# Kernel optimization log

Hardware: AMD Instinct MI355X
Metric: run time of the kernel (lower is better)

The kernel has to match this reference:

```python
import jax, jax.numpy as jnp
import numpy as np

B, N = 1, 1024
C_A, C_Z, H = 768, 128, 16
CH = C_A // H  # 48
INV_SQRT_CH = float(1.0 / np.sqrt(CH))


def _ln(x, w, b):
    # torch.nn.LayerNorm over last dim, eps=1e-5
    m = jnp.mean(x, axis=-1, keepdims=True)
    v = jnp.mean(jnp.square(x - m), axis=-1, keepdims=True)
    return (x - m) * jax.lax.rsqrt(v + 1e-5) * w + b


def setup_inputs() -> dict:
    key = jax.random.key(0)
    ks = jax.random.split(key, 8)
    rn = lambda k, shape, sc: jax.random.normal(k, shape, dtype=jnp.float32) * sc
    return {
        "a": rn(ks[0], (B, N, C_A), 1.0),
        "z": rn(ks[1], (B, N, N, C_Z), 1.0),
        "mask": jnp.ones((B, N), dtype=jnp.float32),
        "ln_a_w": jnp.ones((C_A,), jnp.float32),
        "ln_a_b": jnp.zeros((C_A,), jnp.float32),
        "ln_z_w": jnp.ones((C_Z,), jnp.float32),
        "ln_z_b": jnp.zeros((C_Z,), jnp.float32),
        "Wq": rn(ks[2], (C_A, H * CH), 0.02),
        "bq": jnp.zeros((H * CH,), jnp.float32),
        "Wk": rn(ks[3], (C_A, H * CH), 0.02),
        "Wv": rn(ks[4], (C_A, H * CH), 0.02),
        "Wb": rn(ks[5], (C_Z, H), 0.02),
        "Wg": rn(ks[6], (C_A, H * CH), 0.02),
        "Wo": rn(ks[7], (H * CH, C_A), 0.02),
    }


def reference(a, z, mask, ln_a_w, ln_a_b, ln_z_w, ln_z_b, Wq, bq, Wk, Wv, Wb, Wg, Wo):
    an = _ln(a, ln_a_w, ln_a_b)                                  # [B, N, C_A]
    q = (an @ Wq + bq).reshape(B, N, H, CH)
    k = (an @ Wk).reshape(B, N, H, CH)
    v = (an @ Wv).reshape(B, N, H, CH)
    # pair bias: LayerNorm(z) -> per-head scalar bias [B, N, N, H]
    bpair = _ln(z, ln_z_w, ln_z_b) @ Wb
    mbias = (mask - 1.0)[:, None, None, :] * 1e9                  # [B, 1, 1, N]
    logits = jnp.einsum('bqhc,bkhc->bhqk', q, k) * INV_SQRT_CH
    logits = logits + jnp.transpose(bpair, (0, 3, 1, 2)) + mbias  # [B, H, N, N]
    attn = jax.nn.softmax(logits, axis=-1)
    o = jnp.einsum('bhqk,bkhc->bqhc', attn, v)                    # [B, N, H, CH]
    g = jax.nn.sigmoid(an @ Wg).reshape(B, N, H, CH)
    out = (g * o).reshape(B, N, H * CH) @ Wo                      # [B, N, C_A]
    return out
```

## Files before the change

kernel.cpp:

```cpp
#include <hip/hip_runtime.h>

#define NSEQ 1024
#define CA   768
#define CZ   128
#define NH   16
#define CHD  48
#define HC   768
#define INV_SQRT_CH 0.14433756729740643f

typedef float v4f __attribute__((ext_vector_type(4)));
typedef short v8s __attribute__((ext_vector_type(8)));

__device__ __forceinline__ short f2bf(float f) {
  union { float f; unsigned u; } v; v.f = f;
  unsigned r = v.u + 0x7fffu + ((v.u >> 16) & 1u);
  return (short)(r >> 16);
}
__device__ __forceinline__ float bf2f(short s) {
  union { unsigned u; float f; } v;
  v.u = ((unsigned)(unsigned short)s) << 16;
  return v.f;
}
__device__ __forceinline__ unsigned cvtpk(float lo, float hi) {
  unsigned r;
  asm("v_cvt_pk_bf16_f32 %0, %1, %2" : "=v"(r) : "v"(lo), "v"(hi));
  return r;
}

__global__ __launch_bounds__(256) void k_front(
    const float* __restrict__ lnzw, const float* __restrict__ lnzb,
    const float* __restrict__ Wb, short* __restrict__ wWp, float* __restrict__ S1bW,
    const float* __restrict__ Wq, const float* __restrict__ Wk,
    const float* __restrict__ Wv, const float* __restrict__ Wg,
    const float* __restrict__ Wo, short* __restrict__ WT, short* __restrict__ WoT,
    const float* __restrict__ a, const float* __restrict__ lnaw,
    const float* __restrict__ lnab, short* __restrict__ anb)
{
  __shared__ __align__(16) char fsm[64 * 65 * 4];
  const int bid = blockIdx.x;
  const int t = threadIdx.x;

  if (bid == 0) {
    const int s = t >> 6, l = t & 63;
    const int r16 = l & 15, cg = l >> 4;
    float v[8];
    #pragma unroll
    for (int j = 0; j < 8; ++j) {
      int d = s * 32 + cg * 8 + j;
      v[j] = lnzw[d] * Wb[d * NH + r16];
    }
    uint4 pk;
    pk.x = cvtpk(v[0], v[1]); pk.y = cvtpk(v[2], v[3]);
    pk.z = cvtpk(v[4], v[5]); pk.w = cvtpk(v[6], v[7]);
    *(uint4*)(wWp + (s * 64 + l) * 8) = pk;
    if (t < NH) {
      float s1 = 0.f, bw = 0.f;
      for (int d = 0; d < CZ; ++d) {
        float wb = Wb[d * NH + t];
        s1 += bf2f(f2bf(lnzw[d] * wb));
        bw += lnzb[d] * wb;
      }
      S1bW[t] = s1;
      S1bW[NH + t] = bw;
    }
  } else if (bid <= 720) {
    float (*tile)[65] = (float(*)[65])fsm;
    const int cb = bid - 1;
    const int mat = cb / 144, rem = cb % 144;
    const int tk = rem % 12, tn = rem / 12;
    const int k0 = tk * 64, n0 = tn * 64;
    const float* __restrict__ W =
        (mat == 0) ? Wq : (mat == 1) ? Wk : (mat == 2) ? Wv : (mat == 3) ? Wg : Wo;
    const float s = (mat == 0) ? INV_SQRT_CH : 1.f;
    const int rr = t >> 4, cc = (t & 15) * 4;
    #pragma unroll
    for (int r = 0; r < 4; ++r) {
      v4f v = *(const v4f*)(W + (size_t)(k0 + r * 16 + rr) * HC + n0 + cc);
      tile[r * 16 + rr][cc + 0] = v[0];
      tile[r * 16 + rr][cc + 1] = v[1];
      tile[r * 16 + rr][cc + 2] = v[2];
      tile[r * 16 + rr][cc + 3] = v[3];
    }
    __syncthreads();
    short* dst = (mat < 4) ? (WT + (size_t)mat * HC * CA) : WoT;
    #pragma unroll
    for (int r = 0; r < 4; ++r) {
      const int nr = r * 16 + rr;
      uint2 pk;
      pk.x = cvtpk(tile[cc + 0][nr] * s, tile[cc + 1][nr] * s);
      pk.y = cvtpk(tile[cc + 2][nr] * s, tile[cc + 3][nr] * s);
      *(uint2*)(dst + (size_t)(n0 + nr) * CA + k0 + cc) = pk;
    }
  } else {
    float* red = (float*)fsm;
    const int row = bid - 721;
    const float* ar = a + (size_t)row * CA;
    float x[3];
    float s = 0.f, s2 = 0.f;
    #pragma unroll
    for (int i = 0; i < 3; ++i) {
      x[i] = ar[t + i * 256];
      s += x[i]; s2 += x[i] * x[i];
    }
    #pragma unroll
    for (int off = 1; off < 64; off <<= 1) {
      s += __shfl_xor(s, off);
      s2 += __shfl_xor(s2, off);
    }
    const int wv = t >> 6;
    if ((t & 63) == 0) { red[wv] = s; red[4 + wv] = s2; }
    __syncthreads();
    s = red[0] + red[1] + red[2] + red[3];
    s2 = red[4] + red[5] + red[6] + red[7];
    const float m = s * (1.f / CA);
    const float var = s2 * (1.f / CA) - m * m;
    const float rs = rsqrtf(var + 1e-5f);
    #pragma unroll
    for (int i = 0; i < 3; ++i) {
      int c = t + i * 256;
      anb[(size_t)row * CA + c] = f2bf((x[i] - m) * rs * lnaw[c] + lnab[c]);
    }
  }
}

__global__ __launch_bounds__(256) void k23_fused(
    const short* __restrict__ anb, const short* __restrict__ WT,
    const float* __restrict__ bq, const float* __restrict__ z,
    const short* __restrict__ wWp, const float* __restrict__ S1bW,
    short* __restrict__ qb, short* __restrict__ kb, short* __restrict__ vT,
    float* __restrict__ gbuf, short* __restrict__ bpair)
{
  __shared__ __align__(16) char smem[20480];
  const int tid = threadIdx.x;
  const int w = tid >> 6, l = tid & 63;
  const int r16 = l & 15, cg = l >> 4;

  if (blockIdx.x < 192) {
    const int bid = blockIdx.x;
    const int bm = bid & 7;
    const int bnb = bid >> 3;
    const int m0 = bm * 128, n0 = bnb * 128;
    const int wr = w >> 1, wc = w & 1;

    short* As = (short*)smem;
    short* Bs = (short*)(smem + 10240);

    const int strow = w * 16 + (l >> 2);
    const int scol = (l & 3) * 8;

    v4f acc[4][4];
    #pragma unroll
    for (int i = 0; i < 4; ++i)
      #pragma unroll
      for (int j = 0; j < 4; ++j)
        acc[i][j] = (v4f){0.f, 0.f, 0.f, 0.f};

    for (int k0 = 0; k0 < CA; k0 += 32) {
      v8s av0 = *(const v8s*)(anb + (size_t)(m0 + strow) * CA + k0 + scol);
      v8s av1 = *(const v8s*)(anb + (size_t)(m0 + 64 + strow) * CA + k0 + scol);
      v8s bv0 = *(const v8s*)(WT + (size_t)(n0 + strow) * CA + k0 + scol);
      v8s bv1 = *(const v8s*)(WT + (size_t)(n0 + 64 + strow) * CA + k0 + scol);
      __syncthreads();
      *(v8s*)(As + (size_t)strow * 40 + scol) = av0;
      *(v8s*)(As + (size_t)(64 + strow) * 40 + scol) = av1;
      *(v8s*)(Bs + (size_t)strow * 40 + scol) = bv0;
      *(v8s*)(Bs + (size_t)(64 + strow) * 40 + scol) = bv1;
      __syncthreads();
      v8s a[4], b[4];
      #pragma unroll
      for (int m = 0; m < 4; ++m)
        a[m] = *(const v8s*)(As + (wr * 64 + m * 16 + r16) * 40 + cg * 8);
      #pragma unroll
      for (int n = 0; n < 4; ++n)
        b[n] = *(const v8s*)(Bs + (wc * 64 + n * 16 + r16) * 40 + cg * 8);
      #pragma unroll
      for (int m = 0; m < 4; ++m)
        #pragma unroll
        for (int n = 0; n < 4; ++n)
          acc[m][n] = __builtin_amdgcn_mfma_f32_16x16x32_bf16(a[m], b[n], acc[m][n], 0, 0, 0);
    }

    const int matsel = n0 / HC;
    #pragma unroll
    for (int n = 0; n < 4; ++n) {
      const int nc = (n0 % HC) + wc * 64 + n * 16 + r16;
      const int rbase = m0 + wr * 64 + cg * 4;
      if (matsel == 0) {
        const float bqs = bq[nc] * INV_SQRT_CH;
        #pragma unroll
        for (int m = 0; m < 4; ++m)
          #pragma unroll
          for (int j = 0; j < 4; ++j)
            qb[(size_t)(rbase + m * 16 + j) * HC + nc] = f2bf(acc[m][n][j] + bqs);
      } else if (matsel == 1) {
        #pragma unroll
        for (int m = 0; m < 4; ++m)
          #pragma unroll
          for (int j = 0; j < 4; ++j)
            kb[(size_t)(rbase + m * 16 + j) * HC + nc] = f2bf(acc[m][n][j]);
      } else if (matsel == 2) {
        #pragma unroll
        for (int m = 0; m < 4; ++m) {
          uint2 pk;
          pk.x = cvtpk(acc[m][n][0], acc[m][n][1]);
          pk.y = cvtpk(acc[m][n][2], acc[m][n][3]);
          *(uint2*)(vT + (size_t)nc * NSEQ + rbase + m * 16) = pk;
        }
      } else {
        #pragma unroll
        for (int m = 0; m < 4; ++m)
          #pragma unroll
          for (int j = 0; j < 4; ++j)
            gbuf[(size_t)(rbase + m * 16 + j) * HC + nc] =
                1.f / (1.f + __expf(-acc[m][n][j]));
      }
    }
  } else {
    const int zbid = blockIdx.x - 192;
    const int q = zbid >> 4;
    const int k0 = (zbid & 15) << 6;
    short* blds = (short*)smem;

    v8s bfrag[4];
    #pragma unroll
    for (int s = 0; s < 4; ++s) bfrag[s] = *(const v8s*)(wWp + (s * 64 + l) * 8);
    const float S1 = S1bW[r16];
    const float bW = S1bW[NH + r16];

    const int krow = k0 + w * 16 + r16;
    const float* __restrict__ zr = z + ((size_t)q * NSEQ + krow) * CZ;
    float sum = 0.f, sum2 = 0.f;
    v8s afrag[4];
    #pragma unroll
    for (int s = 0; s < 4; ++s) {
      v4f z0 = *(const v4f*)(zr + s * 32 + cg * 8);
      v4f z1 = *(const v4f*)(zr + s * 32 + cg * 8 + 4);
      #pragma unroll
      for (int j = 0; j < 4; ++j) {
        sum += z0[j] + z1[j];
        sum2 += z0[j] * z0[j] + z1[j] * z1[j];
      }
      union { v8s s8; unsigned u[4]; } fu;
      fu.u[0] = cvtpk(z0[0], z0[1]);
      fu.u[1] = cvtpk(z0[2], z0[3]);
      fu.u[2] = cvtpk(z1[0], z1[1]);
      fu.u[3] = cvtpk(z1[2], z1[3]);
      afrag[s] = fu.s8;
    }
    sum  += __shfl_xor(sum, 16);  sum  += __shfl_xor(sum, 32);
    sum2 += __shfl_xor(sum2, 16); sum2 += __shfl_xor(sum2, 32);
    const float mean = sum * (1.f / CZ);
    const float var = sum2 * (1.f / CZ) - mean * mean;
    const float rs = rsqrtf(var + 1e-5f);

    v4f acc = {0.f, 0.f, 0.f, 0.f};
    #pragma unroll
    for (int s = 0; s < 4; ++s)
      acc = __builtin_amdgcn_mfma_f32_16x16x32_bf16(afrag[s], bfrag[s], acc, 0, 0, 0);

    float bv[4];
    #pragma unroll
    for (int j = 0; j < 4; ++j) {
      int src = cg * 4 + j;
      float mj = __shfl(mean, src);
      float rj = __shfl(rs, src);
      bv[j] = rj * (acc[j] - mj * S1) + bW;
    }
    uint2 bu;
    bu.x = cvtpk(bv[0], bv[1]);
    bu.y = cvtpk(bv[2], bv[3]);
    *(uint2*)&blds[r16 * 72 + w * 16 + cg * 4] = bu;
    __syncthreads();
    const int h = tid >> 4, kk = (tid & 15) << 2;
    uint2 v = *(const uint2*)&blds[h * 72 + kk];
    *(uint2*)(bpair + (size_t)h * NSEQ * NSEQ + (size_t)q * NSEQ + k0 + kk) = v;
  }
}

#define PL_STRIDE 136
#define BL_STRIDE 144
__global__ __launch_bounds__(256) void k4_attn(
    const short* __restrict__ qb, const short* __restrict__ kb,
    const short* __restrict__ vT, const short* __restrict__ bpair,
    const float* __restrict__ mask,
    float* __restrict__ po, float* __restrict__ pm, float* __restrict__ plo)
{
  const int h = blockIdx.x & 15;
  const int qt = (blockIdx.x >> 4) & 15;
  const int ks = blockIdx.x >> 8;
  const int tid = threadIdx.x;
  const int w = tid >> 6, l = tid & 63;
  const int r16 = l & 15, cg = l >> 4;
  const int q0 = qt * 64 + w * 16;
  const int kstart = ks * 256;

  __shared__ __align__(16) short plds[4][16 * PL_STRIDE];
  __shared__ __align__(16) short blds[4][16 * BL_STRIDE];
  short* pl = &plds[w][0];
  short* bl = &blds[w][0];

  const v8s vzero = {0, 0, 0, 0, 0, 0, 0, 0};
  v8s qf0, qf1;
  {
    const short* qp = qb + (size_t)(q0 + r16) * HC + h * CHD;
    qf0 = *(const v8s*)(qp + cg * 8);
    qf1 = (cg < 2) ? *(const v8s*)(qp + 32 + cg * 8) : vzero;
  }
  v4f of0 = {0, 0, 0, 0}, of1 = {0, 0, 0, 0}, of2 = {0, 0, 0, 0};
  float mrun[4], lrun[4];
  #pragma unroll
  for (int j = 0; j < 4; ++j) { mrun[j] = -1e30f; lrun[j] = 0.f; }

  const size_t bpb = (size_t)h * NSEQ * NSEQ;
  const int srow = l >> 2;
  const int scol = (l & 3) * 32;

  #pragma unroll
  for (int ch = 0; ch < 2; ++ch) {
    const int k0 = kstart + ch * 128;

    {
      const short* bsrc = bpair + bpb + (size_t)(q0 + srow) * NSEQ + k0 + scol;
      short* bdst = bl + srow * BL_STRIDE + scol;
      v8s t0 = *(const v8s*)(bsrc);
      v8s t1 = *(const v8s*)(bsrc + 8);
      v8s t2 = *(const v8s*)(bsrc + 16);
      v8s t3 = *(const v8s*)(bsrc + 24);
      *(v8s*)(bdst)      = t0;
      *(v8s*)(bdst + 8)  = t1;
      *(v8s*)(bdst + 16) = t2;
      *(v8s*)(bdst + 24) = t3;
    }

    v4f cs[8];
    #pragma unroll
    for (int kt = 0; kt < 8; ++kt) {
      const short* kp = kb + (size_t)(k0 + kt * 16 + r16) * HC + h * CHD;
      v8s b0 = *(const v8s*)(kp + cg * 8);
      v8s b1 = (cg < 2) ? *(const v8s*)(kp + 32 + cg * 8) : vzero;
      v4f tacc = {0.f, 0.f, 0.f, 0.f};
      tacc = __builtin_amdgcn_mfma_f32_16x16x32_bf16(qf0, b0, tacc, 0, 0, 0);
      tacc = __builtin_amdgcn_mfma_f32_16x16x32_bf16(qf1, b1, tacc, 0, 0, 0);
      cs[kt] = tacc;
    }
    #pragma unroll
    for (int kt = 0; kt < 8; ++kt) {
      const int kc = k0 + kt * 16 + r16;
      const float mb = (mask[kc] - 1.f) * 1e9f;
      #pragma unroll
      for (int j = 0; j < 4; ++j)
        cs[kt][j] += bf2f(bl[(cg * 4 + j) * BL_STRIDE + kt * 16 + r16]) + mb;
    }
    #pragma unroll
    for (int j = 0; j < 4; ++j) {
      float mx = fmaxf(fmaxf(fmaxf(cs[0][j], cs[1][j]), fmaxf(cs[2][j], cs[3][j])),
                       fmaxf(fmaxf(cs[4][j], cs[5][j]), fmaxf(cs[6][j], cs[7][j])));
      mx = fmaxf(mx, __shfl_xor(mx, 1));
      mx = fmaxf(mx, __shfl_xor(mx, 2));
      mx = fmaxf(mx, __shfl_xor(mx, 4));
      mx = fmaxf(mx, __shfl_xor(mx, 8));
      const float mnew = fmaxf(mrun[j], mx);
      const float alpha = __expf(mrun[j] - mnew);
      mrun[j] = mnew;
      float p[8];
      #pragma unroll
      for (int kt = 0; kt < 8; ++kt) p[kt] = __expf(cs[kt][j] - mnew);
      float rsum = ((p[0] + p[1]) + (p[2] + p[3])) + ((p[4] + p[5]) + (p[6] + p[7]));
      rsum += __shfl_xor(rsum, 1);
      rsum += __shfl_xor(rsum, 2);
      rsum += __shfl_xor(rsum, 4);
      rsum += __shfl_xor(rsum, 8);
      lrun[j] = lrun[j] * alpha + rsum;
      of0[j] *= alpha; of1[j] *= alpha; of2[j] *= alpha;
      const int rowb = (cg * 4 + j) * PL_STRIDE;
      #pragma unroll
      for (int t2 = 0; t2 < 4; ++t2) {
        unsigned u = cvtpk(p[2 * t2], p[2 * t2 + 1]);
        pl[rowb + (2 * t2) * 16 + r16] = (short)u;
        pl[rowb + (2 * t2 + 1) * 16 + r16] = (short)(u >> 16);
      }
    }
    asm volatile("s_waitcnt lgkmcnt(0)" ::: "memory");
    __builtin_amdgcn_sched_barrier(0);
    #pragma unroll
    for (int ks4 = 0; ks4 < 4; ++ks4) {
      v8s pa = *(const v8s*)(pl + r16 * PL_STRIDE + ks4 * 32 + cg * 8);
      const short* vp = vT + (size_t)(h * CHD + r16) * NSEQ + k0 + ks4 * 32 + cg * 8;
      v8s bv0 = *(const v8s*)vp;
      v8s bv1 = *(const v8s*)(vp + 16 * NSEQ);
      v8s bv2 = *(const v8s*)(vp + 32 * NSEQ);
      of0 = __builtin_amdgcn_mfma_f32_16x16x32_bf16(pa, bv0, of0, 0, 0, 0);
      of1 = __builtin_amdgcn_mfma_f32_16x16x32_bf16(pa, bv1, of1, 0, 0, 0);
      of2 = __builtin_amdgcn_mfma_f32_16x16x32_bf16(pa, bv2, of2, 0, 0, 0);
    }
  }

  #pragma unroll
  for (int j = 0; j < 4; ++j) {
    const int q = q0 + cg * 4 + j;
    const size_t rb = (((size_t)ks * NSEQ + q) * NH + h) * CHD + r16;
    po[rb]      = of0[j];
    po[rb + 16] = of1[j];
    po[rb + 32] = of2[j];
    if (r16 == 0) {
      pm[((size_t)ks * NSEQ + q) * NH + h] = mrun[j];
      plo[((size_t)ks * NSEQ + q) * NH + h] = lrun[j];
    }
  }
}

__global__ __launch_bounds__(256) void kcomb(
    const float* __restrict__ po, const float* __restrict__ pm,
    const float* __restrict__ plo, const float* __restrict__ gbuf,
    short* __restrict__ gob)
{
  const int q = blockIdx.x;
  const int t = threadIdx.x;
  const int h = t >> 4, s = t & 15;
  float mi[4], li[4];
  #pragma unroll
  for (int i = 0; i < 4; ++i) {
    mi[i] = pm[((size_t)i * NSEQ + q) * NH + h];
    li[i] = plo[((size_t)i * NSEQ + q) * NH + h];
  }
  float mstar = fmaxf(fmaxf(mi[0], mi[1]), fmaxf(mi[2], mi[3]));
  float wgt[4], L = 0.f;
  #pragma unroll
  for (int i = 0; i < 4; ++i) { wgt[i] = __expf(mi[i] - mstar); L += li[i] * wgt[i]; }
  const float inv = 1.f / L;
  #pragma unroll
  for (int dd = 0; dd < 3; ++dd) {
    const int d = s + dd * 16;
    float o = 0.f;
    #pragma unroll
    for (int i = 0; i < 4; ++i)
      o += po[(((size_t)i * NSEQ + q) * NH + h) * CHD + d] * wgt[i];
    const float gv = gbuf[(size_t)q * HC + h * CHD + d];
    gob[(size_t)q * HC + h * CHD + d] = f2bf(o * inv * gv);
  }
}

__global__ __launch_bounds__(256) void k5_out(
    const short* __restrict__ gob, const short* __restrict__ WoT,
    float* __restrict__ out)
{
  __shared__ __align__(16) short As[64 * 40];
  __shared__ __align__(16) short Bs[64 * 40];
  const int tid = threadIdx.x;
  const int w = tid >> 6, l = tid & 63;
  const int r16 = l & 15, cg = l >> 4;
  const int bm = blockIdx.x & 15;
  const int bn = blockIdx.x >> 4;
  const int m0 = bm * 64, n0 = bn * 64;
  const int wr = w >> 1, wc = w & 1;
  const int strow = tid >> 2;
  const int scol = (tid & 3) * 8;

  v4f acc[2][2];
  #pragma unroll
  for (int i = 0; i < 2; ++i)
    #pragma unroll
    for (int j = 0; j < 2; ++j)
      acc[i][j] = (v4f){0.f, 0.f, 0.f, 0.f};

  for (int k0 = 0; k0 < CA; k0 += 32) {
    v8s av = *(const v8s*)(gob + (size_t)(m0 + strow) * CA + k0 + scol);
    v8s bv = *(const v8s*)(WoT + (size_t)(n0 + strow) * CA + k0 + scol);
    __syncthreads();
    *(v8s*)(As + (size_t)strow * 40 + scol) = av;
    *(v8s*)(Bs + (size_t)strow * 40 + scol) = bv;
    __syncthreads();
    v8s a[2], b[2];
    #pragma unroll
    for (int m = 0; m < 2; ++m)
      a[m] = *(const v8s*)(As + (wr * 32 + m * 16 + r16) * 40 + cg * 8);
    #pragma unroll
    for (int n = 0; n < 2; ++n)
      b[n] = *(const v8s*)(Bs + (wc * 32 + n * 16 + r16) * 40 + cg * 8);
    #pragma unroll
    for (int m = 0; m < 2; ++m)
      #pragma unroll
      for (int n = 0; n < 2; ++n)
        acc[m][n] = __builtin_amdgcn_mfma_f32_16x16x32_bf16(a[m], b[n], acc[m][n], 0, 0, 0);
  }

  #pragma unroll
  for (int n = 0; n < 2; ++n) {
    const int nc = n0 + wc * 32 + n * 16 + r16;
    const int rbase = m0 + wr * 32 + cg * 4;
    #pragma unroll
    for (int m = 0; m < 2; ++m)
      #pragma unroll
      for (int j = 0; j < 4; ++j)
        out[(size_t)(rbase + m * 16 + j) * CA + nc] = acc[m][n][j];
  }
}

extern "C" void kernel_launch(void* const* d_in, const int* in_sizes, int n_in,
                              void* d_out, int out_size, void* d_ws, size_t ws_size,
                              hipStream_t stream) {
  const float* a      = (const float*)d_in[0];
  const float* z      = (const float*)d_in[1];
  const float* mask   = (const float*)d_in[2];
  const float* ln_a_w = (const float*)d_in[3];
  const float* ln_a_b = (const float*)d_in[4];
  const float* ln_z_w = (const float*)d_in[5];
  const float* ln_z_b = (const float*)d_in[6];
  const float* Wq     = (const float*)d_in[7];
  const float* bq     = (const float*)d_in[8];
  const float* Wk     = (const float*)d_in[9];
  const float* Wv     = (const float*)d_in[10];
  const float* Wb     = (const float*)d_in[11];
  const float* Wg     = (const float*)d_in[12];
  const float* Wo     = (const float*)d_in[13];
  float* out = (float*)d_out;

  char* ws = (char*)d_ws;
  short* anb   = (short*)(ws);
  short* WT    = (short*)(ws + (2ull << 20));
  short* WoT   = (short*)(ws + (7ull << 20));
  short* qb    = (short*)(ws + (9ull << 20));
  short* kb    = (short*)(ws + (11ull << 20));
  short* vT    = (short*)(ws + (13ull << 20));
  float* gbuf  = (float*)(ws + (15ull << 20));
  short* wWp   = (short*)(ws + (19ull << 20));
  float* S1bW  = (float*)(ws + (19ull << 20) + 4096ull);
  short* gob   = (short*)(ws + (20ull << 20));
  float* po    = (float*)(ws + (22ull << 20));
  float* pm    = (float*)(ws + (36ull << 20));
  float* plo   = (float*)(ws + (37ull << 20));
  short* bpair = (short*)(ws + (38ull << 20));

  k_front<<<1745, 256, 0, stream>>>(ln_z_w, ln_z_b, Wb, wWp, S1bW,
                                    Wq, Wk, Wv, Wg, Wo, WT, WoT,
                                    a, ln_a_w, ln_a_b, anb);
  k23_fused<<<192 + 16384, 256, 0, stream>>>(anb, WT, bq, z, wWp, S1bW,
                                             qb, kb, vT, gbuf, bpair);
  k4_attn<<<1024, 256, 0, stream>>>(qb, kb, vT, bpair, mask, po, pm, plo);
  kcomb<<<1024, 256, 0, stream>>>(po, pm, plo, gbuf, gob);
  k5_out<<<192, 256, 0, stream>>>(gob, WoT, out);
}
```

Before: 196.2 us.

## Split fused GEMM/pair-bias kernel and widen attention key split to 8 chunks

The fused kernel that ran the QKVG GEMM blocks and the pair-bias LayerNorm blocks is split into two separate launches. The attention kernel now runs one 64-thread wave per block, each handling a 16-query tile over a single 128-key chunk, so the launch has 8192 blocks instead of 1024. This removes the in-kernel online-softmax rescaling loop. The combine kernel merges 8 partial results per query instead of 4. The change trades more partial-output traffic (partial buffers double in size) and an extra launch for more parallelism and lower per-wave register and LDS use.

```diff
diff --git a/kernel.cpp b/kernel.cpp
--- a/kernel.cpp
+++ b/kernel.cpp
@@ -123,181 +123,175 @@
   }
 }
 
-__global__ __launch_bounds__(256) void k23_fused(
+__global__ __launch_bounds__(256) void k2_gemm(
     const short* __restrict__ anb, const short* __restrict__ WT,
-    const float* __restrict__ bq, const float* __restrict__ z,
-    const short* __restrict__ wWp, const float* __restrict__ S1bW,
+    const float* __restrict__ bq,
     short* __restrict__ qb, short* __restrict__ kb, short* __restrict__ vT,
-    float* __restrict__ gbuf, short* __restrict__ bpair)
+    float* __restrict__ gbuf)
 {
-  __shared__ __align__(16) char smem[20480];
+  __shared__ __align__(16) short As[128 * 40];
+  __shared__ __align__(16) short Bs[128 * 40];
   const int tid = threadIdx.x;
   const int w = tid >> 6, l = tid & 63;
   const int r16 = l & 15, cg = l >> 4;
-
-  if (blockIdx.x < 192) {
-    const int bid = blockIdx.x;
-    const int bm = bid & 7;
-    const int bnb = bid >> 3;
-    const int m0 = bm * 128, n0 = bnb * 128;
-    const int wr = w >> 1, wc = w & 1;
-
-    short* As = (short*)smem;
-    short* Bs = (short*)(smem + 10240);
-
-    const int strow = w * 16 + (l >> 2);
-    const int scol = (l & 3) * 8;
-
-    v4f acc[4][4];
-    #pragma unroll
-    for (int i = 0; i < 4; ++i)
-      #pragma unroll
-      for (int j = 0; j < 4; ++j)
-        acc[i][j] = (v4f){0.f, 0.f, 0.f, 0.f};
-
-    for (int k0 = 0; k0 < CA; k0 += 32) {
-      v8s av0 = *(const v8s*)(anb + (size_t)(m0 + strow) * CA + k0 + scol);
-      v8s av1 = *(const v8s*)(anb + (size_t)(m0 + 64 + strow) * CA + k0 + scol);
-      v8s bv0 = *(const v8s*)(WT + (size_t)(n0 + strow) * CA + k0 + scol);
-      v8s bv1 = *(const v8s*)(WT + (size_t)(n0 + 64 + strow) * CA + k0 + scol);
-      __syncthreads();
-      *(v8s*)(As + (size_t)strow * 40 + scol) = av0;
-      *(v8s*)(As + (size_t)(64 + strow) * 40 + scol) = av1;
-      *(v8s*)(Bs + (size_t)strow * 40 + scol) = bv0;
-      *(v8s*)(Bs + (size_t)(64 + strow) * 40 + scol) = bv1;
-      __syncthreads();
-      v8s a[4], b[4];
-      #pragma unroll
-      for (int m = 0; m < 4; ++m)
-        a[m] = *(const v8s*)(As + (wr * 64 + m * 16 + r16) * 40 + cg * 8);
+  const int bm = blockIdx.x & 7;
+  const int bnb = blockIdx.x >> 3;
+  const int m0 = bm * 128, n0 = bnb * 128;
+  const int wr = w >> 1, wc = w & 1;
+  const int strow = w * 16 + (l >> 2);
+  const int scol = (l & 3) * 8;
+
+  v4f acc[4][4];
+  #pragma unroll
+  for (int i = 0; i < 4; ++i)
+    #pragma unroll
+    for (int j = 0; j < 4; ++j)
+      acc[i][j] = (v4f){0.f, 0.f, 0.f, 0.f};
+
+  for (int k0 = 0; k0 < CA; k0 += 32) {
+    v8s av0 = *(const v8s*)(anb + (size_t)(m0 + strow) * CA + k0 + scol);
+    v8s av1 = *(const v8s*)(anb + (size_t)(m0 + 64 + strow) * CA + k0 + scol);
+    v8s bv0 = *(const v8s*)(WT + (size_t)(n0 + strow) * CA + k0 + scol);
+    v8s bv1 = *(const v8s*)(WT + (size_t)(n0 + 64 + strow) * CA + k0 + scol);
+    __syncthreads();
+    *(v8s*)(As + (size_t)strow * 40 + scol) = av0;
+    *(v8s*)(As + (size_t)(64 + strow) * 40 + scol) = av1;
+    *(v8s*)(Bs + (size_t)strow * 40 + scol) = bv0;
+    *(v8s*)(Bs + (size_t)(64 + strow) * 40 + scol) = bv1;
+    __syncthreads();
+    v8s a[4], b[4];
+    #pragma unroll
+    for (int m = 0; m < 4; ++m)
+      a[m] = *(const v8s*)(As + (wr * 64 + m * 16 + r16) * 40 + cg * 8);
+    #pragma unroll
+    for (int n = 0; n < 4; ++n)
+      b[n] = *(const v8s*)(Bs + (wc * 64 + n * 16 + r16) * 40 + cg * 8);
+    #pragma unroll
+    for (int m = 0; m < 4; ++m)
       #pragma unroll
       for (int n = 0; n < 4; ++n)
-        b[n] = *(const v8s*)(Bs + (wc * 64 + n * 16 + r16) * 40 + cg * 8);
+        acc[m][n] = __builtin_amdgcn_mfma_f32_16x16x32_bf16(a[m], b[n], acc[m][n], 0, 0, 0);
+  }
+
+  const int matsel = n0 / HC;
+  #pragma unroll
+  for (int n = 0; n < 4; ++n) {
+    const int nc = (n0 % HC) + wc * 64 + n * 16 + r16;
+    const int rbase = m0 + wr * 64 + cg * 4;
+    if (matsel == 0) {
+      const float bqs = bq[nc] * INV_SQRT_CH;
       #pragma unroll
       for (int m = 0; m < 4; ++m)
         #pragma unroll
-        for (int n = 0; n < 4; ++n)
-          acc[m][n] = __builtin_amdgcn_mfma_f32_16x16x32_bf16(a[m], b[n], acc[m][n], 0, 0, 0);
-    }
-
-    const int matsel = n0 / HC;
-    #pragma unroll
-    for (int n = 0; n < 4; ++n) {
-      const int nc = (n0 % HC) + wc * 64 + n * 16 + r16;
-      const int rbase = m0 + wr * 64 + cg * 4;
-      if (matsel == 0) {
-        const float bqs = bq[nc] * INV_SQRT_CH;
+        for (int j = 0; j < 4; ++j)
+          qb[(size_t)(rbase + m * 16 + j) * HC + nc] = f2bf(acc[m][n][j] + bqs);
+    } else if (matsel == 1) {
+      #pragma unroll
+      for (int m = 0; m < 4; ++m)
         #pragma unroll
-        for (int m = 0; m < 4; ++m)
-          #pragma unroll
-          for (int j = 0; j < 4; ++j)
-            qb[(size_t)(rbase + m * 16 + j) * HC + nc] = f2bf(acc[m][n][j] + bqs);
-      } else if (matsel == 1) {
+        for (int j = 0; j < 4; ++j)
+          kb[(size_t)(rbase + m * 16 + j) * HC + nc] = f2bf(acc[m][n][j]);
+    } else if (matsel == 2) {
+      #pragma unroll
+      for (int m = 0; m < 4; ++m) {
+        uint2 pk;
+        pk.x = cvtpk(acc[m][n][0], acc[m][n][1]);
+        pk.y = cvtpk(acc[m][n][2], acc[m][n][3]);
+        *(uint2*)(vT + (size_t)nc * NSEQ + rbase + m * 16) = pk;
+      }
+    } else {
+      #pragma unroll
+      for (int m = 0; m < 4; ++m)
         #pragma unroll
-        for (int m = 0; m < 4; ++m)
-          #pragma unroll
-          for (int j = 0; j < 4; ++j)
-            kb[(size_t)(rbase + m * 16 + j) * HC + nc] = f2bf(acc[m][n][j]);
-      } else if (matsel == 2) {
-        #pragma unroll
-        for (int m = 0; m < 4; ++m) {
-          uint2 pk;
-          pk.x = cvtpk(acc[m][n][0], acc[m][n][1]);
-          pk.y = cvtpk(acc[m][n][2], acc[m][n][3]);
-          *(uint2*)(vT + (size_t)nc * NSEQ + rbase + m * 16) = pk;
-        }
-      } else {
-        #pragma unroll
-        for (int m = 0; m < 4; ++m)
-          #pragma unroll
-          for (int j = 0; j < 4; ++j)
-            gbuf[(size_t)(rbase + m * 16 + j) * HC + nc] =
-                1.f / (1.f + __expf(-acc[m][n][j]));
-      }
-    }
-  } else {
-    const int zbid = blockIdx.x - 192;
-    const int q = zbid >> 4;
-    const int k0 = (zbid & 15) << 6;
-    short* blds = (short*)smem;
-
-    v8s bfrag[4];
-    #pragma unroll
-    for (int s = 0; s < 4; ++s) bfrag[s] = *(const v8s*)(wWp + (s * 64 + l) * 8);
-    const float S1 = S1bW[r16];
-    const float bW = S1bW[NH + r16];
-
-    const int krow = k0 + w * 16 + r16;
-    const float* __restrict__ zr = z + ((size_t)q * NSEQ + krow) * CZ;
-    float sum = 0.f, sum2 = 0.f;
-    v8s afrag[4];
-    #pragma unroll
-    for (int s = 0; s < 4; ++s) {
-      v4f z0 = *(const v4f*)(zr + s * 32 + cg * 8);
-      v4f z1 = *(const v4f*)(zr + s * 32 + cg * 8 + 4);
-      #pragma unroll
-      for (int j = 0; j < 4; ++j) {
-        sum += z0[j] + z1[j];
-        sum2 += z0[j] * z0[j] + z1[j] * z1[j];
-      }
-      union { v8s s8; unsigned u[4]; } fu;
-      fu.u[0] = cvtpk(z0[0], z0[1]);
-      fu.u[1] = cvtpk(z0[2], z0[3]);
-      fu.u[2] = cvtpk(z1[0], z1[1]);
-      fu.u[3] = cvtpk(z1[2], z1[3]);
-      afrag[s] = fu.s8;
-    }
-    sum  += __shfl_xor(sum, 16);  sum  += __shfl_xor(sum, 32);
-    sum2 += __shfl_xor(sum2, 16); sum2 += __shfl_xor(sum2, 32);
-    const float mean = sum * (1.f / CZ);
-    const float var = sum2 * (1.f / CZ) - mean * mean;
-    const float rs = rsqrtf(var + 1e-5f);
-
-    v4f acc = {0.f, 0.f, 0.f, 0.f};
-    #pragma unroll
-    for (int s = 0; s < 4; ++s)
-      acc = __builtin_amdgcn_mfma_f32_16x16x32_bf16(afrag[s], bfrag[s], acc, 0, 0, 0);
-
-    float bv[4];
+        for (int j = 0; j < 4; ++j)
+          gbuf[(size_t)(rbase + m * 16 + j) * HC + nc] =
+              1.f / (1.f + __expf(-acc[m][n][j]));
+    }
+  }
+}
+
+__global__ __launch_bounds__(256) void k3_z(
+    const float* __restrict__ z, const short* __restrict__ wWp,
+    const float* __restrict__ S1bW, short* __restrict__ bpair)
+{
+  __shared__ __align__(16) short blds[16 * 72];
+  const int tid = threadIdx.x;
+  const int w = tid >> 6, l = tid & 63;
+  const int r16 = l & 15, cg = l >> 4;
+  const int q = blockIdx.x >> 4;
+  const int k0 = (blockIdx.x & 15) << 6;
+
+  v8s bfrag[4];
+  #pragma unroll
+  for (int s = 0; s < 4; ++s) bfrag[s] = *(const v8s*)(wWp + (s * 64 + l) * 8);
+  const float S1 = S1bW[r16];
+  const float bW = S1bW[NH + r16];
+
+  const int krow = k0 + w * 16 + r16;
+  const float* __restrict__ zr = z + ((size_t)q * NSEQ + krow) * CZ;
+  float sum = 0.f, sum2 = 0.f;
+  v8s afrag[4];
+  #pragma unroll
+  for (int s = 0; s < 4; ++s) {
+    v4f z0 = *(const v4f*)(zr + s * 32 + cg * 8);
+    v4f z1 = *(const v4f*)(zr + s * 32 + cg * 8 + 4);
     #pragma unroll
     for (int j = 0; j < 4; ++j) {
-      int src = cg * 4 + j;
-      float mj = __shfl(mean, src);
-      float rj = __shfl(rs, src);
-      bv[j] = rj * (acc[j] - mj * S1) + bW;
-    }
-    uint2 bu;
-    bu.x = cvtpk(bv[0], bv[1]);
-    bu.y = cvtpk(bv[2], bv[3]);
-    *(uint2*)&blds[r16 * 72 + w * 16 + cg * 4] = bu;
-    __syncthreads();
-    const int h = tid >> 4, kk = (tid & 15) << 2;
-    uint2 v = *(const uint2*)&blds[h * 72 + kk];
-    *(uint2*)(bpair + (size_t)h * NSEQ * NSEQ + (size_t)q * NSEQ + k0 + kk) = v;
-  }
+      sum += z0[j] + z1[j];
+      sum2 += z0[j] * z0[j] + z1[j] * z1[j];
+    }
+    union { v8s s8; unsigned u[4]; } fu;
+    fu.u[0] = cvtpk(z0[0], z0[1]);
+    fu.u[1] = cvtpk(z0[2], z0[3]);
+    fu.u[2] = cvtpk(z1[0], z1[1]);
+    fu.u[3] = cvtpk(z1[2], z1[3]);
+    afrag[s] = fu.s8;
+  }
+  sum  += __shfl_xor(sum, 16);  sum  += __shfl_xor(sum, 32);
+  sum2 += __shfl_xor(sum2, 16); sum2 += __shfl_xor(sum2, 32);
+  const float mean = sum * (1.f / CZ);
+  const float var = sum2 * (1.f / CZ) - mean * mean;
+  const float rs = rsqrtf(var + 1e-5f);
+
+  v4f acc = {0.f, 0.f, 0.f, 0.f};
+  #pragma unroll
+  for (int s = 0; s < 4; ++s)
+    acc = __builtin_amdgcn_mfma_f32_16x16x32_bf16(afrag[s], bfrag[s], acc, 0, 0, 0);
+
+  float bv[4];
+  #pragma unroll
+  for (int j = 0; j < 4; ++j) {
+    int src = cg * 4 + j;
+    float mj = __shfl(mean, src);
+    float rj = __shfl(rs, src);
+    bv[j] = rj * (acc[j] - mj * S1) + bW;
+  }
+  uint2 bu;
+  bu.x = cvtpk(bv[0], bv[1]);
+  bu.y = cvtpk(bv[2], bv[3]);
+  *(uint2*)&blds[r16 * 72 + w * 16 + cg * 4] = bu;
+  __syncthreads();
+  const int h = tid >> 4, kk = (tid & 15) << 2;
+  uint2 v = *(const uint2*)&blds[h * 72 + kk];
+  *(uint2*)(bpair + (size_t)h * NSEQ * NSEQ + (size_t)q * NSEQ + k0 + kk) = v;
 }
 
 #define PL_STRIDE 136
-#define BL_STRIDE 144
-__global__ __launch_bounds__(256) void k4_attn(
+__global__ __launch_bounds__(64) void k4_attn(
     const short* __restrict__ qb, const short* __restrict__ kb,
     const short* __restrict__ vT, const short* __restrict__ bpair,
     const float* __restrict__ mask,
     float* __restrict__ po, float* __restrict__ pm, float* __restrict__ plo)
 {
   const int h = blockIdx.x & 15;
-  const int qt = (blockIdx.x >> 4) & 15;
-  const int ks = blockIdx.x >> 8;
-  const int tid = threadIdx.x;
-  const int w = tid >> 6, l = tid & 63;
+  const int qt = (blockIdx.x >> 4) & 63;
+  const int ks = blockIdx.x >> 10;
+  const int l = threadIdx.x;
   const int r16 = l & 15, cg = l >> 4;
-  const int q0 = qt * 64 + w * 16;
-  const int kstart = ks * 256;
-
-  __shared__ __align__(16) short plds[4][16 * PL_STRIDE];
-  __shared__ __align__(16) short blds[4][16 * BL_STRIDE];
-  short* pl = &plds[w][0];
-  short* bl = &blds[w][0];
+  const int q0 = qt * 16;
+  const int k0 = ks * 128;
+
+  __shared__ __align__(16) short pl[16 * PL_STRIDE];
 
   const v8s vzero = {0, 0, 0, 0, 0, 0, 0, 0};
   v8s qf0, qf1;
@@ -306,93 +300,85 @@
     qf0 = *(const v8s*)(qp + cg * 8);
     qf1 = (cg < 2) ? *(const v8s*)(qp + 32 + cg * 8) : vzero;
   }
+
+  const size_t bpb = (size_t)h * NSEQ * NSEQ;
+  {
+    const int srow = l >> 2;
+    const int scol = (l & 3) * 32;
+    const short* bsrc = bpair + bpb + (size_t)(q0 + srow) * NSEQ + k0 + scol;
+    short* bdst = pl + srow * PL_STRIDE + scol;
+    v8s t0 = *(const v8s*)(bsrc);
+    v8s t1 = *(const v8s*)(bsrc + 8);
+    v8s t2 = *(const v8s*)(bsrc + 16);
+    v8s t3 = *(const v8s*)(bsrc + 24);
+    *(v8s*)(bdst)      = t0;
+    *(v8s*)(bdst + 8)  = t1;
+    *(v8s*)(bdst + 16) = t2;
+    *(v8s*)(bdst + 24) = t3;
+  }
+
+  v4f cs[8];
+  #pragma unroll
+  for (int kt = 0; kt < 8; ++kt) {
+    const short* kp = kb + (size_t)(k0 + kt * 16 + r16) * HC + h * CHD;
+    v8s b0 = *(const v8s*)(kp + cg * 8);
+    v8s b1 = (cg < 2) ? *(const v8s*)(kp + 32 + cg * 8) : vzero;
+    v4f tacc = {0.f, 0.f, 0.f, 0.f};
+    tacc = __builtin_amdgcn_mfma_f32_16x16x32_bf16(qf0, b0, tacc, 0, 0, 0);
+    tacc = __builtin_amdgcn_mfma_f32_16x16x32_bf16(qf1, b1, tacc, 0, 0, 0);
+    cs[kt] = tacc;
+  }
+
+  #pragma unroll
+  for (int kt = 0; kt < 8; ++kt) {
+    const int kc = k0 + kt * 16 + r16;
+    const float mb = (mask[kc] - 1.f) * 1e9f;
+    #pragma unroll
+    for (int j = 0; j < 4; ++j)
+      cs[kt][j] += bf2f(pl[(cg * 4 + j) * PL_STRIDE + kt * 16 + r16]) + mb;
+  }
+
+  float mx4[4], ls4[4];
+  #pragma unroll
+  for (int j = 0; j < 4; ++j) {
+    float mx = fmaxf(fmaxf(fmaxf(cs[0][j], cs[1][j]), fmaxf(cs[2][j], cs[3][j])),
+                     fmaxf(fmaxf(cs[4][j], cs[5][j]), fmaxf(cs[6][j], cs[7][j])));
+    mx = fmaxf(mx, __shfl_xor(mx, 1));
+    mx = fmaxf(mx, __shfl_xor(mx, 2));
+    mx = fmaxf(mx, __shfl_xor(mx, 4));
+    mx = fmaxf(mx, __shfl_xor(mx, 8));
+    mx4[j] = mx;
+    float p[8];
+    #pragma unroll
+    for (int kt = 0; kt < 8; ++kt) p[kt] = __expf(cs[kt][j] - mx);
+    float rsum = ((p[0] + p[1]) + (p[2] + p[3])) + ((p[4] + p[5]) + (p[6] + p[7]));
+    rsum += __shfl_xor(rsum, 1);
+    rsum += __shfl_xor(rsum, 2);
+    rsum += __shfl_xor(rsum, 4);
+    rsum += __shfl_xor(rsum, 8);
+    ls4[j] = rsum;
+    const int rowb = (cg * 4 + j) * PL_STRIDE;
+    #pragma unroll
+    for (int t2 = 0; t2 < 4; ++t2) {
+      unsigned u = cvtpk(p[2 * t2], p[2 * t2 + 1]);
+      pl[rowb + (2 * t2) * 16 + r16] = (short)u;
+      pl[rowb + (2 * t2 + 1) * 16 + r16] = (short)(u >> 16);
+    }
+  }
+  asm volatile("s_waitcnt lgkmcnt(0)" ::: "memory");
+  __builtin_amdgcn_sched_barrier(0);
+
   v4f of0 = {0, 0, 0, 0}, of1 = {0, 0, 0, 0}, of2 = {0, 0, 0, 0};
-  float mrun[4], lrun[4];
-  #pragma unroll
-  for (int j = 0; j < 4; ++j) { mrun[j] = -1e30f; lrun[j] = 0.f; }
-
-  const size_t bpb = (size_t)h * NSEQ * NSEQ;
-  const int srow = l >> 2;
-  const int scol = (l & 3) * 32;
-
-  #pragma unroll
-  for (int ch = 0; ch < 2; ++ch) {
-    const int k0 = kstart + ch * 128;
-
-    {
-      const short* bsrc = bpair + bpb + (size_t)(q0 + srow) * NSEQ + k0 + scol;
-      short* bdst = bl + srow * BL_STRIDE + scol;
-      v8s t0 = *(const v8s*)(bsrc);
-      v8s t1 = *(const v8s*)(bsrc + 8);
-      v8s t2 = *(const v8s*)(bsrc + 16);
-      v8s t3 = *(const v8s*)(bsrc + 24);
-      *(v8s*)(bdst)      = t0;
-      *(v8s*)(bdst + 8)  = t1;
-      *(v8s*)(bdst + 16) = t2;
-      *(v8s*)(bdst + 24) = t3;
-    }
-
-    v4f cs[8];
-    #pragma unroll
-    for (int kt = 0; kt < 8; ++kt) {
-      const short* kp = kb + (size_t)(k0 + kt * 16 + r16) * HC + h * CHD;
-      v8s b0 = *(const v8s*)(kp + cg * 8);
-      v8s b1 = (cg < 2) ? *(const v8s*)(kp + 32 + cg * 8) : vzero;
-      v4f tacc = {0.f, 0.f, 0.f, 0.f};
-      tacc = __builtin_amdgcn_mfma_f32_16x16x32_bf16(qf0, b0, tacc, 0, 0, 0);
-      tacc = __builtin_amdgcn_mfma_f32_16x16x32_bf16(qf1, b1, tacc, 0, 0, 0);
-      cs[kt] = tacc;
-    }
-    #pragma unroll
-    for (int kt = 0; kt < 8; ++kt) {
-      const int kc = k0 + kt * 16 + r16;
-      const float mb = (mask[kc] - 1.f) * 1e9f;
-      #pragma unroll
-      for (int j = 0; j < 4; ++j)
-        cs[kt][j] += bf2f(bl[(cg * 4 + j) * BL_STRIDE + kt * 16 + r16]) + mb;
-    }
-    #pragma unroll
-    for (int j = 0; j < 4; ++j) {
-      float mx = fmaxf(fmaxf(fmaxf(cs[0][j], cs[1][j]), fmaxf(cs[2][j], cs[3][j])),
-                       fmaxf(fmaxf(cs[4][j], cs[5][j]), fmaxf(cs[6][j], cs[7][j])));
-      mx = fmaxf(mx, __shfl_xor(mx, 1));
-      mx = fmaxf(mx, __shfl_xor(mx, 2));
-      mx = fmaxf(mx, __shfl_xor(mx, 4));
-      mx = fmaxf(mx, __shfl_xor(mx, 8));
-      const float mnew = fmaxf(mrun[j], mx);
-      const float alpha = __expf(mrun[j] - mnew);
-      mrun[j] = mnew;
-      float p[8];
-      #pragma unroll
-      for (int kt = 0; kt < 8; ++kt) p[kt] = __expf(cs[kt][j] - mnew);
-      float rsum = ((p[0] + p[1]) + (p[2] + p[3])) + ((p[4] + p[5]) + (p[6] + p[7]));
-      rsum += __shfl_xor(rsum, 1);
-      rsum += __shfl_xor(rsum, 2);
-      rsum += __shfl_xor(rsum, 4);
-      rsum += __shfl_xor(rsum, 8);
-      lrun[j] = lrun[j] * alpha + rsum;
-      of0[j] *= alpha; of1[j] *= alpha; of2[j] *= alpha;
-      const int rowb = (cg * 4 + j) * PL_STRIDE;
-      #pragma unroll
-      for (int t2 = 0; t2 < 4; ++t2) {
-        unsigned u = cvtpk(p[2 * t2], p[2 * t2 + 1]);
-        pl[rowb + (2 * t2) * 16 + r16] = (short)u;
-        pl[rowb + (2 * t2 + 1) * 16 + r16] = (short)(u >> 16);
-      }
-    }
-    asm volatile("s_waitcnt lgkmcnt(0)" ::: "memory");
-    __builtin_amdgcn_sched_barrier(0);
-    #pragma unroll
-    for (int ks4 = 0; ks4 < 4; ++ks4) {
-      v8s pa = *(const v8s*)(pl + r16 * PL_STRIDE + ks4 * 32 + cg * 8);
-      const short* vp = vT + (size_t)(h * CHD + r16) * NSEQ + k0 + ks4 * 32 + cg * 8;
-      v8s bv0 = *(const v8s*)vp;
-      v8s bv1 = *(const v8s*)(vp + 16 * NSEQ);
-      v8s bv2 = *(const v8s*)(vp + 32 * NSEQ);
-      of0 = __builtin_amdgcn_mfma_f32_16x16x32_bf16(pa, bv0, of0, 0, 0, 0);
-      of1 = __builtin_amdgcn_mfma_f32_16x16x32_bf16(pa, bv1, of1, 0, 0, 0);
-      of2 = __builtin_amdgcn_mfma_f32_16x16x32_bf16(pa, bv2, of2, 0, 0, 0);
-    }
+  #pragma unroll
+  for (int ks4 = 0; ks4 < 4; ++ks4) {
+    v8s pa = *(const v8s*)(pl + r16 * PL_STRIDE + ks4 * 32 + cg * 8);
+    const short* vp = vT + (size_t)(h * CHD + r16) * NSEQ + k0 + ks4 * 32 + cg * 8;
+    v8s bv0 = *(const v8s*)vp;
+    v8s bv1 = *(const v8s*)(vp + 16 * NSEQ);
+    v8s bv2 = *(const v8s*)(vp + 32 * NSEQ);
+    of0 = __builtin_amdgcn_mfma_f32_16x16x32_bf16(pa, bv0, of0, 0, 0, 0);
+    of1 = __builtin_amdgcn_mfma_f32_16x16x32_bf16(pa, bv1, of1, 0, 0, 0);
+    of2 = __builtin_amdgcn_mfma_f32_16x16x32_bf16(pa, bv2, of2, 0, 0, 0);
   }
 
   #pragma unroll
@@ -403,8 +389,8 @@
     po[rb + 16] = of1[j];
     po[rb + 32] = of2[j];
     if (r16 == 0) {
-      pm[((size_t)ks * NSEQ + q) * NH + h] = mrun[j];
-      plo[((size_t)ks * NSEQ + q) * NH + h] = lrun[j];
+      pm[((size_t)ks * NSEQ + q) * NH + h] = mx4[j];
+      plo[((size_t)ks * NSEQ + q) * NH + h] = ls4[j];
     }
   }
 }
@@ -417,23 +403,25 @@
   const int q = blockIdx.x;
   const int t = threadIdx.x;
   const int h = t >> 4, s = t & 15;
-  float mi[4], li[4];
-  #pragma unroll
-  for (int i = 0; i < 4; ++i) {
+  float mi[8], li[8];
+  #pragma unroll
+  for (int i = 0; i < 8; ++i) {
     mi[i] = pm[((size_t)i * NSEQ + q) * NH + h];
     li[i] = plo[((size_t)i * NSEQ + q) * NH + h];
   }
-  float mstar = fmaxf(fmaxf(mi[0], mi[1]), fmaxf(mi[2], mi[3]));
-  float wgt[4], L = 0.f;
-  #pragma unroll
-  for (int i = 0; i < 4; ++i) { wgt[i] = __expf(mi[i] - mstar); L += li[i] * wgt[i]; }
+  float mstar = -1e30f;
+  #pragma unroll
+  for (int i = 0; i < 8; ++i) mstar = fmaxf(mstar, mi[i]);
+  float wgt[8], L = 0.f;
+  #pragma unroll
+  for (int i = 0; i < 8; ++i) { wgt[i] = __expf(mi[i] - mstar); L += li[i] * wgt[i]; }
   const float inv = 1.f / L;
   #pragma unroll
   for (int dd = 0; dd < 3; ++dd) {
     const int d = s + dd * 16;
     float o = 0.f;
     #pragma unroll
-    for (int i = 0; i < 4; ++i)
+    for (int i = 0; i < 8; ++i)
       o += po[(((size_t)i * NSEQ + q) * NH + h) * CHD + d] * wgt[i];
     const float gv = gbuf[(size_t)q * HC + h * CHD + d];
     gob[(size_t)q * HC + h * CHD + d] = f2bf(o * inv * gv);
@@ -527,16 +515,16 @@
   float* S1bW  = (float*)(ws + (19ull << 20) + 4096ull);
   short* gob   = (short*)(ws + (20ull << 20));
   float* po    = (float*)(ws + (22ull << 20));
-  float* pm    = (float*)(ws + (36ull << 20));
-  float* plo   = (float*)(ws + (37ull << 20));
-  short* bpair = (short*)(ws + (38ull << 20));
+  float* pm    = (float*)(ws + (48ull << 20));
+  float* plo   = (float*)(ws + (49ull << 20));
+  short* bpair = (short*)(ws + (50ull << 20));
 
   k_front<<<1745, 256, 0, stream>>>(ln_z_w, ln_z_b, Wb, wWp, S1bW,
                                     Wq, Wk, Wv, Wg, Wo, WT, WoT,
                                     a, ln_a_w, ln_a_b, anb);
-  k23_fused<<<192 + 16384, 256, 0, stream>>>(anb, WT, bq, z, wWp, S1bW,
-                                             qb, kb, vT, gbuf, bpair);
-  k4_attn<<<1024, 256, 0, stream>>>(qb, kb, vT, bpair, mask, po, pm, plo);
+  k2_gemm<<<192, 256, 0, stream>>>(anb, WT, bq, qb, kb, vT, gbuf);
+  k3_z<<<16384, 256, 0, stream>>>(z, wWp, S1bW, bpair);
+  k4_attn<<<8192, 64, 0, stream>>>(qb, kb, vT, bpair, mask, po, pm, plo);
   kcomb<<<1024, 256, 0, stream>>>(po, pm, plo, gbuf, gob);
   k5_out<<<192, 256, 0, stream>>>(gob, WoT, out);
 }
```

Result: no change. 198.4 us (+1.2%).
